# Performance work log

Measured on AMD Instinct MI355X. Metric: run time of the kernel, lower is better.

Reference implementation:

```python
import jax, jax.numpy as jnp
import numpy as np

N_NODES = 50000
N_EDGES = 800000
NFEAT, NHID, NCLASS = 512, 256, 128
N_UV = 2048


def gcn_layer(x, adj_row, adj_col, adj_val, W, b):
    # support = x @ W ; out = A @ support (sparse COO spmm) + b
    support = x @ W                                   # [N, out]
    msgs = adj_val[:, None] * support[adj_col]        # [E, out]
    out = jax.ops.segment_sum(msgs, adj_row, num_segments=N_NODES)
    return out + b


def setup_inputs() -> dict:
    key = jax.random.key(0)
    ks = jax.random.split(key, 12)
    u = jax.random.randint(ks[0], (N_UV,), 0, N_NODES)
    v = jax.random.randint(ks[1], (N_UV,), 0, N_NODES)
    x = jax.random.normal(ks[2], (N_NODES, NFEAT), dtype=jnp.float32)
    adj_row = jnp.sort(jax.random.randint(ks[3], (N_EDGES,), 0, N_NODES))
    adj_col = jax.random.randint(ks[4], (N_EDGES,), 0, N_NODES)
    adj_val = jax.random.uniform(ks[5], (N_EDGES,), dtype=jnp.float32)
    s1 = 1.0 / np.sqrt(NHID)
    s2 = 1.0 / np.sqrt(NCLASS)
    W1 = jax.random.uniform(ks[6], (NFEAT, NHID), minval=-s1, maxval=s1, dtype=jnp.float32)
    b1 = jax.random.uniform(ks[7], (NHID,), minval=-s1, maxval=s1, dtype=jnp.float32)
    W2 = jax.random.uniform(ks[8], (NHID, NCLASS), minval=-s2, maxval=s2, dtype=jnp.float32)
    b2 = jax.random.uniform(ks[9], (NCLASS,), minval=-s2, maxval=s2, dtype=jnp.float32)
    We = jax.random.normal(ks[10], (NCLASS, NCLASS), dtype=jnp.float32) * (1.0 / np.sqrt(NCLASS))
    return {"u": u, "v": v, "x": x, "adj_row": adj_row, "adj_col": adj_col,
            "adj_val": adj_val, "W1": W1, "b1": b1, "W2": W2, "b2": b2, "We": We}


def reference(u, v, x, adj_row, adj_col, adj_val, W1, b1, W2, b2, We):
    # layer 1: GCN + ReLU (dropout is identity in eval mode)
    h = jax.nn.relu(gcn_layer(x, adj_row, adj_col, adj_val, W1, b1))
    # layer 2: GCN
    z = gcn_layer(h, adj_row, adj_col, adj_val, W2, b2)          # [N, nclass]
    # edge scoring: sigmoid(w_edge(z[u]) @ z[v].T)
    zu = z[u] @ We.T                                             # [U, nclass] (nn.Linear: x @ W.T)
    zv = z[v]                                                    # [V, nclass]
    p_uv = jax.nn.sigmoid(zu @ zv.T)                             # [U, V]
    return p_uv
```

## Files before the change

### kernel.cpp

```cpp
#include <hip/hip_runtime.h>
#include <hip/hip_bf16.h>
#include <math.h>

#define N_NODES 50000
#define N_EDGES 800000
#define NFEAT   512
#define NHID    256
#define NCLASS  128
#define N_UV    2048

typedef __bf16    bf16x8 __attribute__((ext_vector_type(8)));
typedef short     s16x8  __attribute__((ext_vector_type(8)));
typedef float     f32x4  __attribute__((ext_vector_type(4)));

__device__ __forceinline__ unsigned short bf16_rn(float f) {
  unsigned u = __float_as_uint(f);
  u += 0x7fffu + ((u >> 16) & 1u);
  return (unsigned short)(u >> 16);
}
__device__ __forceinline__ float bf16_to_f(unsigned short h) {
  return __uint_as_float(((unsigned)h) << 16);
}

#define LDSPAD 40

template <bool ASPLIT, bool BSPLIT, bool SIGMOID, bool AIDX, bool BIDX>
__global__ __launch_bounds__(256, 2) void gemm_mfma_split(
    const float* __restrict__ Af,
    const unsigned short* __restrict__ Ahi, const unsigned short* __restrict__ Alo,
    const int* __restrict__ Aidx,
    const float* __restrict__ BTf,
    const unsigned short* __restrict__ BThi, const unsigned short* __restrict__ BTlo,
    const int* __restrict__ Bidx,
    float* __restrict__ C, int M, int N, int K) {
  __shared__ unsigned short sAh[128 * LDSPAD];
  __shared__ unsigned short sAl[128 * LDSPAD];
  __shared__ unsigned short sBh[128 * LDSPAD];
  __shared__ unsigned short sBl[128 * LDSPAD];

  const int tid  = threadIdx.x;
  const int lane = tid & 63;
  const int wave = tid >> 6;
  const int wm   = (wave >> 1) << 6;
  const int wn   = (wave & 1) << 6;
  const int lm   = lane & 15;
  const int quad = lane >> 4;
  const int m0   = blockIdx.y * 128;
  const int n0   = blockIdx.x * 128;

  const int r32 = tid >> 3;
  const int c32 = (tid & 7) * 4;
  const int r16 = tid >> 2;
  const int c16 = (tid & 3) * 8;

  float4 pA[4]; s16x8 pAh[2], pAl[2];
  float4 pB[4]; s16x8 pBh[2], pBl[2];

  f32x4 acc[4][4];
#pragma unroll
  for (int i = 0; i < 4; ++i)
#pragma unroll
    for (int j = 0; j < 4; ++j)
#pragma unroll
      for (int r = 0; r < 4; ++r) acc[i][j][r] = 0.f;

#define LOAD_TILE(k0)                                                          \
  do {                                                                         \
    if (ASPLIT) {                                                              \
      _Pragma("unroll") for (int p = 0; p < 4; ++p) {                          \
        const int m = m0 + p * 32 + r32;                                       \
        pA[p] = make_float4(0.f, 0.f, 0.f, 0.f);                               \
        if (m < M) {                                                           \
          const int ra = AIDX ? Aidx[m] : m;                                   \
          pA[p] = *(const float4*)&Af[(size_t)ra * K + (k0) + c32];            \
        }                                                                      \
      }                                                                        \
    } else {                                                                   \
      _Pragma("unroll") for (int p = 0; p < 2; ++p) {                          \
        const int m = m0 + p * 64 + r16;                                       \
        _Pragma("unroll") for (int e = 0; e < 8; ++e) { pAh[p][e] = 0; pAl[p][e] = 0; } \
        if (m < M) {                                                           \
          pAh[p] = *(const s16x8*)&Ahi[(size_t)m * K + (k0) + c16];            \
          pAl[p] = *(const s16x8*)&Alo[(size_t)m * K + (k0) + c16];            \
        }                                                                      \
      }                                                                        \
    }                                                                          \
    if (BSPLIT) {                                                              \
      _Pragma("unroll") for (int p = 0; p < 4; ++p) {                          \
        const int n = n0 + p * 32 + r32;                                       \
        const int rb = BIDX ? Bidx[n] : n;                                     \
        pB[p] = *(const float4*)&BTf[(size_t)rb * K + (k0) + c32];             \
      }                                                                        \
    } else {                                                                   \
      _Pragma("unroll") for (int p = 0; p < 2; ++p) {                          \
        pBh[p] = *(const s16x8*)&BThi[(size_t)(n0 + p * 64 + r16) * K + (k0) + c16]; \
        pBl[p] = *(const s16x8*)&BTlo[(size_t)(n0 + p * 64 + r16) * K + (k0) + c16]; \
      }                                                                        \
    }                                                                          \
  } while (0)

#define SPLIT4(v, hv, lv)                                                      \
  hv.x = bf16_rn(v.x); lv.x = bf16_rn(v.x - bf16_to_f(hv.x));                  \
  hv.y = bf16_rn(v.y); lv.y = bf16_rn(v.y - bf16_to_f(hv.y));                  \
  hv.z = bf16_rn(v.z); lv.z = bf16_rn(v.z - bf16_to_f(hv.z));                  \
  hv.w = bf16_rn(v.w); lv.w = bf16_rn(v.w - bf16_to_f(hv.w));

#define STORE_TILE()                                                           \
  do {                                                                         \
    if (ASPLIT) {                                                              \
      _Pragma("unroll") for (int p = 0; p < 4; ++p) {                          \
        ushort4 hv, lv; SPLIT4(pA[p], hv, lv);                                 \
        const int row = p * 32 + r32;                                          \
        *(ushort4*)&sAh[row * LDSPAD + c32] = hv;                              \
        *(ushort4*)&sAl[row * LDSPAD + c32] = lv;                              \
      }                                                                        \
    } else {                                                                   \
      _Pragma("unroll") for (int p = 0; p < 2; ++p) {                          \
        const int row = p * 64 + r16;                                          \
        *(s16x8*)&sAh[row * LDSPAD + c16] = pAh[p];                            \
        *(s16x8*)&sAl[row * LDSPAD + c16] = pAl[p];                            \
      }                                                                        \
    }                                                                          \
    if (BSPLIT) {                                                              \
      _Pragma("unroll") for (int p = 0; p < 4; ++p) {                          \
        ushort4 hv, lv; SPLIT4(pB[p], hv, lv);                                 \
        const int row = p * 32 + r32;                                          \
        *(ushort4*)&sBh[row * LDSPAD + c32] = hv;                              \
        *(ushort4*)&sBl[row * LDSPAD + c32] = lv;                              \
      }                                                                        \
    } else {                                                                   \
      _Pragma("unroll") for (int p = 0; p < 2; ++p) {                          \
        const int row = p * 64 + r16;                                          \
        *(s16x8*)&sBh[row * LDSPAD + c16] = pBh[p];                            \
        *(s16x8*)&sBl[row * LDSPAD + c16] = pBl[p];                            \
      }                                                                        \
    }                                                                          \
  } while (0)

  LOAD_TILE(0);

  for (int k0 = 0; k0 < K; k0 += 32) {
    if (k0) __syncthreads();
    STORE_TILE();
    __syncthreads();
    if (k0 + 32 < K) LOAD_TILE(k0 + 32);

    bf16x8 aH[4], aL[4], bH[4], bL[4];
#pragma unroll
    for (int i = 0; i < 4; ++i) {
      const int r = wm + i * 16 + lm;
      aH[i] = __builtin_bit_cast(bf16x8, *(const s16x8*)&sAh[r * LDSPAD + quad * 8]);
      aL[i] = __builtin_bit_cast(bf16x8, *(const s16x8*)&sAl[r * LDSPAD + quad * 8]);
    }
#pragma unroll
    for (int j = 0; j < 4; ++j) {
      const int r = wn + j * 16 + lm;
      bH[j] = __builtin_bit_cast(bf16x8, *(const s16x8*)&sBh[r * LDSPAD + quad * 8]);
      bL[j] = __builtin_bit_cast(bf16x8, *(const s16x8*)&sBl[r * LDSPAD + quad * 8]);
    }
#pragma unroll
    for (int i = 0; i < 4; ++i)
#pragma unroll
      for (int j = 0; j < 4; ++j) {
        acc[i][j] = __builtin_amdgcn_mfma_f32_16x16x32_bf16(aH[i], bH[j], acc[i][j], 0, 0, 0);
        acc[i][j] = __builtin_amdgcn_mfma_f32_16x16x32_bf16(aH[i], bL[j], acc[i][j], 0, 0, 0);
        acc[i][j] = __builtin_amdgcn_mfma_f32_16x16x32_bf16(aL[i], bH[j], acc[i][j], 0, 0, 0);
      }
  }

#pragma unroll
  for (int i = 0; i < 4; ++i)
#pragma unroll
    for (int j = 0; j < 4; ++j) {
      const int col = n0 + wn + j * 16 + lm;
#pragma unroll
      for (int r = 0; r < 4; ++r) {
        const int row = m0 + wm + i * 16 + quad * 4 + r;
        if (row < M) {
          float v = acc[i][j][r];
          if (SIGMOID) v = 1.f / (1.f + expf(-v));
          C[(size_t)row * N + col] = v;
        }
      }
    }
#undef LOAD_TILE
#undef STORE_TILE
#undef SPLIT4
}

__global__ __launch_bounds__(256) void prep_all(
    const int* __restrict__ rows, int* __restrict__ row_ptr,
    const float* __restrict__ W1, unsigned short* __restrict__ W1Thi,
    unsigned short* __restrict__ W1Tlo,
    const float* __restrict__ W2, unsigned short* __restrict__ W2Thi,
    unsigned short* __restrict__ W2Tlo) {
  const int idx = blockIdx.x * 256 + threadIdx.x;
  if (idx < N_EDGES) {
    const int r = rows[idx];
    const int rprev = (idx == 0) ? -1 : rows[idx - 1];
    for (int n = rprev + 1; n <= r; ++n) row_ptr[n] = idx;
    if (idx == N_EDGES - 1)
      for (int n = r + 1; n <= N_NODES; ++n) row_ptr[n] = N_EDGES;
  }
  if (idx < NFEAT * NHID) {
    const int n = idx / NFEAT;
    const int k = idx - n * NFEAT;
    const float f = W1[(size_t)k * NHID + n];
    const unsigned short h = bf16_rn(f);
    W1Thi[idx] = h;
    W1Tlo[idx] = bf16_rn(f - bf16_to_f(h));
  }
  if (idx < NHID * NCLASS) {
    const int n = idx / NHID;
    const int k = idx - n * NHID;
    const float f = W2[(size_t)k * NCLASS + n];
    const unsigned short h = bf16_rn(f);
    W2Thi[idx] = h;
    W2Tlo[idx] = bf16_rn(f - bf16_to_f(h));
  }
}

__global__ __launch_bounds__(256) void spmm256_split(
    const float4* __restrict__ S4, const int* __restrict__ row_ptr,
    const int* __restrict__ cols, const float* __restrict__ vals,
    const float4* __restrict__ bias4,
    unsigned short* __restrict__ outHi, unsigned short* __restrict__ outLo) {
  const int wave = threadIdx.x >> 6;
  const int lane = threadIdx.x & 63;
  const int node = blockIdx.x * 4 + wave;

  const int lo = row_ptr[node];
  const int hi = row_ptr[node + 1];

  float4 acc = make_float4(0.f, 0.f, 0.f, 0.f);
  int e = lo;
  for (; e + 8 <= hi; e += 8) {
    int c[8]; float w[8];
#pragma unroll
    for (int t = 0; t < 8; ++t) { c[t] = cols[e + t]; w[t] = vals[e + t]; }
    float4 r[8];
#pragma unroll
    for (int t = 0; t < 8; ++t) r[t] = S4[(size_t)c[t] * 64 + lane];
#pragma unroll
    for (int t = 0; t < 8; ++t) {
      acc.x = fmaf(w[t], r[t].x, acc.x); acc.y = fmaf(w[t], r[t].y, acc.y);
      acc.z = fmaf(w[t], r[t].z, acc.z); acc.w = fmaf(w[t], r[t].w, acc.w);
    }
  }
  for (; e < hi; ++e) {
    const int c = cols[e];
    const float w = vals[e];
    const float4 r = S4[(size_t)c * 64 + lane];
    acc.x = fmaf(w, r.x, acc.x); acc.y = fmaf(w, r.y, acc.y);
    acc.z = fmaf(w, r.z, acc.z); acc.w = fmaf(w, r.w, acc.w);
  }

  const float4 b = bias4[lane];
  acc.x = fmaxf(acc.x + b.x, 0.f);
  acc.y = fmaxf(acc.y + b.y, 0.f);
  acc.z = fmaxf(acc.z + b.z, 0.f);
  acc.w = fmaxf(acc.w + b.w, 0.f);

  ushort4 hv, lv;
  hv.x = bf16_rn(acc.x); lv.x = bf16_rn(acc.x - bf16_to_f(hv.x));
  hv.y = bf16_rn(acc.y); lv.y = bf16_rn(acc.y - bf16_to_f(hv.y));
  hv.z = bf16_rn(acc.z); lv.z = bf16_rn(acc.z - bf16_to_f(hv.z));
  hv.w = bf16_rn(acc.w); lv.w = bf16_rn(acc.w - bf16_to_f(hv.w));
  const size_t o = (size_t)node * NHID + lane * 4;
  *(ushort4*)&outHi[o] = hv;
  *(ushort4*)&outLo[o] = lv;
}

__global__ __launch_bounds__(256) void spmm128_f32(
    const float4* __restrict__ S4, const int* __restrict__ row_ptr,
    const int* __restrict__ cols, const float* __restrict__ vals,
    const float4* __restrict__ bias4, float4* __restrict__ out4) {
  const int wave = threadIdx.x >> 6;
  const int lane = threadIdx.x & 63;
  const int half = lane >> 5;
  const int l32  = lane & 31;
  const int node = blockIdx.x * 4 + wave;

  const int lo = row_ptr[node];
  const int hi = row_ptr[node + 1];

  float4 acc = make_float4(0.f, 0.f, 0.f, 0.f);
  int e = lo + half;
  for (; e + 6 < hi; e += 8) {
    int c[4]; float w[4];
#pragma unroll
    for (int t = 0; t < 4; ++t) { c[t] = cols[e + 2 * t]; w[t] = vals[e + 2 * t]; }
    float4 r[4];
#pragma unroll
    for (int t = 0; t < 4; ++t) r[t] = S4[(size_t)c[t] * 32 + l32];
#pragma unroll
    for (int t = 0; t < 4; ++t) {
      acc.x = fmaf(w[t], r[t].x, acc.x); acc.y = fmaf(w[t], r[t].y, acc.y);
      acc.z = fmaf(w[t], r[t].z, acc.z); acc.w = fmaf(w[t], r[t].w, acc.w);
    }
  }
  for (; e < hi; e += 2) {
    const int c = cols[e];
    const float w = vals[e];
    const float4 r = S4[(size_t)c * 32 + l32];
    acc.x = fmaf(w, r.x, acc.x); acc.y = fmaf(w, r.y, acc.y);
    acc.z = fmaf(w, r.z, acc.z); acc.w = fmaf(w, r.w, acc.w);
  }

  acc.x += __shfl_xor(acc.x, 32);
  acc.y += __shfl_xor(acc.y, 32);
  acc.z += __shfl_xor(acc.z, 32);
  acc.w += __shfl_xor(acc.w, 32);

  if (half == 0) {
    const float4 b = bias4[l32];
    acc.x += b.x; acc.y += b.y; acc.z += b.z; acc.w += b.w;
    out4[(size_t)node * 32 + l32] = acc;
  }
}

extern "C" void kernel_launch(void* const* d_in, const int* in_sizes, int n_in,
                              void* d_out, int out_size, void* d_ws, size_t ws_size,
                              hipStream_t stream) {
  const int*   u       = (const int*)  d_in[0];
  const int*   v       = (const int*)  d_in[1];
  const float* x       = (const float*)d_in[2];
  const int*   adj_row = (const int*)  d_in[3];
  const int*   adj_col = (const int*)  d_in[4];
  const float* adj_val = (const float*)d_in[5];
  const float* W1      = (const float*)d_in[6];
  const float* b1      = (const float*)d_in[7];
  const float* W2      = (const float*)d_in[8];
  const float* b2      = (const float*)d_in[9];
  const float* We      = (const float*)d_in[10];
  float* out = (float*)d_out;

  char* wsb = (char*)d_ws;
  float* S1 = (float*)wsb;
  float* S2 = (float*)wsb;
  float* Z  = (float*)(wsb + (size_t)N_NODES * NCLASS * sizeof(float));
  char* rB = wsb + (size_t)N_NODES * NHID * sizeof(float);
  unsigned short* Hhi = (unsigned short*)rB;
  unsigned short* Hlo = Hhi + (size_t)N_NODES * NHID;
  float* ZU = (float*)rB;
  unsigned short* W1Thi = (unsigned short*)out;
  unsigned short* W1Tlo = W1Thi + NHID * NFEAT;
  unsigned short* W2Thi = W1Tlo + NHID * NFEAT;
  unsigned short* W2Tlo = W2Thi + NCLASS * NHID;
  int* row_ptr = (int*)(W2Tlo + NCLASS * NHID);

  prep_all<<<(N_EDGES + 255) / 256, 256, 0, stream>>>(
      adj_row, row_ptr, W1, W1Thi, W1Tlo, W2, W2Thi, W2Tlo);

  gemm_mfma_split<true, false, false, false, false>
      <<<dim3(NHID / 128, (N_NODES + 127) / 128), 256, 0, stream>>>(
      x, nullptr, nullptr, nullptr, nullptr, W1Thi, W1Tlo, nullptr,
      S1, N_NODES, NHID, NFEAT);

  spmm256_split<<<N_NODES / 4, 256, 0, stream>>>(
      (const float4*)S1, row_ptr, adj_col, adj_val, (const float4*)b1, Hhi, Hlo);

  gemm_mfma_split<false, false, false, false, false>
      <<<dim3(NCLASS / 128, (N_NODES + 127) / 128), 256, 0, stream>>>(
      nullptr, Hhi, Hlo, nullptr, nullptr, W2Thi, W2Tlo, nullptr,
      S2, N_NODES, NCLASS, NHID);

  spmm128_f32<<<N_NODES / 4, 256, 0, stream>>>(
      (const float4*)S2, row_ptr, adj_col, adj_val, (const float4*)b2, (float4*)Z);

  gemm_mfma_split<true, true, false, true, false>
      <<<dim3(NCLASS / 128, N_UV / 128), 256, 0, stream>>>(
      Z, nullptr, nullptr, u, We, nullptr, nullptr, nullptr,
      ZU, N_UV, NCLASS, NCLASS);

  gemm_mfma_split<true, true, true, false, true>
      <<<dim3(N_UV / 128, N_UV / 128), 256, 0, stream>>>(
      ZU, nullptr, nullptr, nullptr, Z, nullptr, nullptr, v,
      out, N_UV, N_UV, NCLASS);
}
```

Baseline: 422.0 us.

## Store GEMM support outputs as 24-bit fixed point to cut SpMM gather traffic

Both support matrices (x@W1 and h@W2) are now written as packed 24-bit signed fixed-point values with a fixed scale instead of fp32. The SpMM kernels gather 12-byte packed groups and unpack them to floats, folding the scale into the edge weight. This cuts the bytes moved by the bandwidth-bound random gathers by a quarter. In exchange it adds unpack ALU work, unaligned 12-byte loads and byte-wise scattered stores in the GEMM epilogue, and it risks clamping or precision loss if values exceed the fixed range.

```diff
diff --git a/kernel.cpp b/kernel.cpp
--- a/kernel.cpp
+++ b/kernel.cpp
@@ -9,9 +9,14 @@
 #define NCLASS  128
 #define N_UV    2048
 
+#define Q24_SCALE  524288.0f
+#define Q24_INV    1.9073486328125e-6f
+
 typedef __bf16    bf16x8 __attribute__((ext_vector_type(8)));
 typedef short     s16x8  __attribute__((ext_vector_type(8)));
 typedef float     f32x4  __attribute__((ext_vector_type(4)));
+
+struct __attribute__((packed)) U3 { unsigned a, b, c; };
 
 __device__ __forceinline__ unsigned short bf16_rn(float f) {
   unsigned u = __float_as_uint(f);
@@ -21,10 +26,24 @@
 __device__ __forceinline__ float bf16_to_f(unsigned short h) {
   return __uint_as_float(((unsigned)h) << 16);
 }
+__device__ __forceinline__ void unpack24(unsigned a, unsigned b, unsigned c,
+                                         int& e0, int& e1, int& e2, int& e3) {
+  e0 = ((int)(a << 8)) >> 8;
+  e1 = ((int)((b << 16) | ((a >> 24) << 8))) >> 8;
+  e2 = ((int)((c << 24) | ((b >> 16) << 8))) >> 8;
+  e3 = ((int)c) >> 8;
+}
+__device__ __forceinline__ void pack24(float v, unsigned char* p) {
+  int q = __float2int_rn(v * Q24_SCALE);
+  q = q > 8388607 ? 8388607 : (q < -8388608 ? -8388608 : q);
+  p[0] = (unsigned char)(q & 0xFF);
+  p[1] = (unsigned char)((q >> 8) & 0xFF);
+  p[2] = (unsigned char)((q >> 16) & 0xFF);
+}
 
 #define LDSPAD 40
 
-template <bool ASPLIT, bool BSPLIT, bool SIGMOID, bool AIDX, bool BIDX>
+template <bool ASPLIT, bool BSPLIT, int OMODE, bool AIDX, bool BIDX>
 __global__ __launch_bounds__(256, 2) void gemm_mfma_split(
     const float* __restrict__ Af,
     const unsigned short* __restrict__ Ahi, const unsigned short* __restrict__ Alo,
@@ -32,7 +51,7 @@
     const float* __restrict__ BTf,
     const unsigned short* __restrict__ BThi, const unsigned short* __restrict__ BTlo,
     const int* __restrict__ Bidx,
-    float* __restrict__ C, int M, int N, int K) {
+    float* __restrict__ C, unsigned char* __restrict__ Cq, int M, int N, int K) {
   __shared__ unsigned short sAh[128 * LDSPAD];
   __shared__ unsigned short sAl[128 * LDSPAD];
   __shared__ unsigned short sBh[128 * LDSPAD];
@@ -178,8 +197,14 @@
         const int row = m0 + wm + i * 16 + quad * 4 + r;
         if (row < M) {
           float v = acc[i][j][r];
-          if (SIGMOID) v = 1.f / (1.f + expf(-v));
-          C[(size_t)row * N + col] = v;
+          if (OMODE == 1) {
+            v = 1.f / (1.f + expf(-v));
+            C[(size_t)row * N + col] = v;
+          } else if (OMODE == 2) {
+            pack24(v, Cq + ((size_t)row * N + col) * 3);
+          } else {
+            C[(size_t)row * N + col] = v;
+          }
         }
       }
     }
@@ -220,8 +245,8 @@
   }
 }
 
-__global__ __launch_bounds__(256) void spmm256_split(
-    const float4* __restrict__ S4, const int* __restrict__ row_ptr,
+__global__ __launch_bounds__(256) void spmm256_q24_split(
+    const unsigned char* __restrict__ Sq, const int* __restrict__ row_ptr,
     const int* __restrict__ cols, const float* __restrict__ vals,
     const float4* __restrict__ bias4,
     unsigned short* __restrict__ outHi, unsigned short* __restrict__ outLo) {
@@ -233,27 +258,35 @@
   const int hi = row_ptr[node + 1];
 
   float4 acc = make_float4(0.f, 0.f, 0.f, 0.f);
+
+#define ACCQ(dd, ww)                                                           \
+  do {                                                                         \
+    int e0, e1, e2, e3;                                                        \
+    unpack24((dd).a, (dd).b, (dd).c, e0, e1, e2, e3);                          \
+    const float ws = (ww) * Q24_INV;                                           \
+    acc.x = fmaf(ws, (float)e0, acc.x);                                        \
+    acc.y = fmaf(ws, (float)e1, acc.y);                                        \
+    acc.z = fmaf(ws, (float)e2, acc.z);                                        \
+    acc.w = fmaf(ws, (float)e3, acc.w);                                        \
+  } while (0)
+
   int e = lo;
   for (; e + 8 <= hi; e += 8) {
     int c[8]; float w[8];
 #pragma unroll
     for (int t = 0; t < 8; ++t) { c[t] = cols[e + t]; w[t] = vals[e + t]; }
-    float4 r[8];
-#pragma unroll
-    for (int t = 0; t < 8; ++t) r[t] = S4[(size_t)c[t] * 64 + lane];
-#pragma unroll
-    for (int t = 0; t < 8; ++t) {
-      acc.x = fmaf(w[t], r[t].x, acc.x); acc.y = fmaf(w[t], r[t].y, acc.y);
-      acc.z = fmaf(w[t], r[t].z, acc.z); acc.w = fmaf(w[t], r[t].w, acc.w);
-    }
+    U3 d[8];
+#pragma unroll
+    for (int t = 0; t < 8; ++t)
+      d[t] = *(const U3*)&Sq[(size_t)c[t] * (NHID * 3) + lane * 12];
+#pragma unroll
+    for (int t = 0; t < 8; ++t) ACCQ(d[t], w[t]);
   }
   for (; e < hi; ++e) {
-    const int c = cols[e];
-    const float w = vals[e];
-    const float4 r = S4[(size_t)c * 64 + lane];
-    acc.x = fmaf(w, r.x, acc.x); acc.y = fmaf(w, r.y, acc.y);
-    acc.z = fmaf(w, r.z, acc.z); acc.w = fmaf(w, r.w, acc.w);
-  }
+    const U3 d = *(const U3*)&Sq[(size_t)cols[e] * (NHID * 3) + lane * 12];
+    ACCQ(d, vals[e]);
+  }
+#undef ACCQ
 
   const float4 b = bias4[lane];
   acc.x = fmaxf(acc.x + b.x, 0.f);
@@ -271,10 +304,10 @@
   *(ushort4*)&outLo[o] = lv;
 }
 
-__global__ __launch_bounds__(256) void spmm128_f32(
-    const float4* __restrict__ S4, const int* __restrict__ row_ptr,
+__global__ __launch_bounds__(256) void spmm128_q24(
+    const unsigned char* __restrict__ Sq, const int* __restrict__ row_ptr,
     const int* __restrict__ cols, const float* __restrict__ vals,
-    const float4* __restrict__ bias4, float4* __restrict__ out4) {
+    const float* __restrict__ bias, float* __restrict__ Z) {
   const int wave = threadIdx.x >> 6;
   const int lane = threadIdx.x & 63;
   const int half = lane >> 5;
@@ -284,38 +317,47 @@
   const int lo = row_ptr[node];
   const int hi = row_ptr[node + 1];
 
-  float4 acc = make_float4(0.f, 0.f, 0.f, 0.f);
+  float acc[4] = {0.f, 0.f, 0.f, 0.f};
+
+#define ACCQ(dd, ww)                                                           \
+  do {                                                                         \
+    int e0, e1, e2, e3;                                                        \
+    unpack24((dd).a, (dd).b, (dd).c, e0, e1, e2, e3);                          \
+    const float ws = (ww) * Q24_INV;                                           \
+    acc[0] = fmaf(ws, (float)e0, acc[0]);                                      \
+    acc[1] = fmaf(ws, (float)e1, acc[1]);                                      \
+    acc[2] = fmaf(ws, (float)e2, acc[2]);                                      \
+    acc[3] = fmaf(ws, (float)e3, acc[3]);                                      \
+  } while (0)
+
   int e = lo + half;
   for (; e + 6 < hi; e += 8) {
     int c[4]; float w[4];
 #pragma unroll
     for (int t = 0; t < 4; ++t) { c[t] = cols[e + 2 * t]; w[t] = vals[e + 2 * t]; }
-    float4 r[4];
-#pragma unroll
-    for (int t = 0; t < 4; ++t) r[t] = S4[(size_t)c[t] * 32 + l32];
-#pragma unroll
-    for (int t = 0; t < 4; ++t) {
-      acc.x = fmaf(w[t], r[t].x, acc.x); acc.y = fmaf(w[t], r[t].y, acc.y);
-      acc.z = fmaf(w[t], r[t].z, acc.z); acc.w = fmaf(w[t], r[t].w, acc.w);
-    }
+    U3 d[4];
+#pragma unroll
+    for (int t = 0; t < 4; ++t)
+      d[t] = *(const U3*)&Sq[(size_t)c[t] * (NCLASS * 3) + l32 * 12];
+#pragma unroll
+    for (int t = 0; t < 4; ++t) ACCQ(d[t], w[t]);
   }
   for (; e < hi; e += 2) {
-    const int c = cols[e];
-    const float w = vals[e];
-    const float4 r = S4[(size_t)c * 32 + l32];
-    acc.x = fmaf(w, r.x, acc.x); acc.y = fmaf(w, r.y, acc.y);
-    acc.z = fmaf(w, r.z, acc.z); acc.w = fmaf(w, r.w, acc.w);
-  }
-
-  acc.x += __shfl_xor(acc.x, 32);
-  acc.y += __shfl_xor(acc.y, 32);
-  acc.z += __shfl_xor(acc.z, 32);
-  acc.w += __shfl_xor(acc.w, 32);
+    const U3 d = *(const U3*)&Sq[(size_t)cols[e] * (NCLASS * 3) + l32 * 12];
+    ACCQ(d, vals[e]);
+  }
+#undef ACCQ
+
+#pragma unroll
+  for (int k = 0; k < 4; ++k) acc[k] += __shfl_xor(acc[k], 32);
 
   if (half == 0) {
-    const float4 b = bias4[l32];
-    acc.x += b.x; acc.y += b.y; acc.z += b.z; acc.w += b.w;
-    out4[(size_t)node * 32 + l32] = acc;
+    float4 v;
+    v.x = acc[0] + bias[l32 * 4 + 0];
+    v.y = acc[1] + bias[l32 * 4 + 1];
+    v.z = acc[2] + bias[l32 * 4 + 2];
+    v.w = acc[3] + bias[l32 * 4 + 3];
+    *(float4*)&Z[(size_t)node * NCLASS + l32 * 4] = v;
   }
 }
 
@@ -336,9 +378,9 @@
   float* out = (float*)d_out;
 
   char* wsb = (char*)d_ws;
-  float* S1 = (float*)wsb;
-  float* S2 = (float*)wsb;
-  float* Z  = (float*)(wsb + (size_t)N_NODES * NCLASS * sizeof(float));
+  unsigned char* S1q = (unsigned char*)wsb;
+  unsigned char* S2q = (unsigned char*)wsb;
+  float* Z = (float*)(wsb + (size_t)N_NODES * NCLASS * 3);
   char* rB = wsb + (size_t)N_NODES * NHID * sizeof(float);
   unsigned short* Hhi = (unsigned short*)rB;
   unsigned short* Hlo = Hhi + (size_t)N_NODES * NHID;
@@ -352,29 +394,29 @@
   prep_all<<<(N_EDGES + 255) / 256, 256, 0, stream>>>(
       adj_row, row_ptr, W1, W1Thi, W1Tlo, W2, W2Thi, W2Tlo);
 
-  gemm_mfma_split<true, false, false, false, false>
+  gemm_mfma_split<true, false, 2, false, false>
       <<<dim3(NHID / 128, (N_NODES + 127) / 128), 256, 0, stream>>>(
       x, nullptr, nullptr, nullptr, nullptr, W1Thi, W1Tlo, nullptr,
-      S1, N_NODES, NHID, NFEAT);
-
-  spmm256_split<<<N_NODES / 4, 256, 0, stream>>>(
-      (const float4*)S1, row_ptr, adj_col, adj_val, (const float4*)b1, Hhi, Hlo);
-
-  gemm_mfma_split<false, false, false, false, false>
+      nullptr, S1q, N_NODES, NHID, NFEAT);
+
+  spmm256_q24_split<<<N_NODES / 4, 256, 0, stream>>>(
+      S1q, row_ptr, adj_col, adj_val, (const float4*)b1, Hhi, Hlo);
+
+  gemm_mfma_split<false, false, 2, false, false>
       <<<dim3(NCLASS / 128, (N_NODES + 127) / 128), 256, 0, stream>>>(
       nullptr, Hhi, Hlo, nullptr, nullptr, W2Thi, W2Tlo, nullptr,
-      S2, N_NODES, NCLASS, NHID);
-
-  spmm128_f32<<<N_NODES / 4, 256, 0, stream>>>(
-      (const float4*)S2, row_ptr, adj_col, adj_val, (const float4*)b2, (float4*)Z);
-
-  gemm_mfma_split<true, true, false, true, false>
+      nullptr, S2q, N_NODES, NCLASS, NHID);
+
+  spmm128_q24<<<N_NODES / 4, 256, 0, stream>>>(
+      S2q, row_ptr, adj_col, adj_val, b2, Z);
+
+  gemm_mfma_split<true, true, 0, true, false>
       <<<dim3(NCLASS / 128, N_UV / 128), 256, 0, stream>>>(
       Z, nullptr, nullptr, u, We, nullptr, nullptr, nullptr,
-      ZU, N_UV, NCLASS, NCLASS);
-
-  gemm_mfma_split<true, true, true, false, true>
+      ZU, nullptr, N_UV, NCLASS, NCLASS);
+
+  gemm_mfma_split<true, true, 1, false, true>
       <<<dim3(N_UV / 128, N_UV / 128), 256, 0, stream>>>(
       ZU, nullptr, nullptr, nullptr, Z, nullptr, nullptr, v,
-      out, N_UV, N_UV, NCLASS);
-}
+      out, nullptr, N_UV, N_UV, NCLASS);
+}
```

Measured after the change: 398.9 us. 5.5% less time.

## Quantize layer-1 support to 24-bit planes and aggregate layer 2 only for u/v nodes

Applied to the files above, without the earlier changes.

The layer-1 GEMM now writes its output as 24-bit fixed-point values split across three byte planes instead of fp32. The layer-1 SpMM gathers these narrower planes, which cuts gather traffic by a quarter. The layer-2 SpMM now runs only for the 4096 nodes indexed by u and v instead of all 50000, and writes a compact ZUV buffer that the final GEMMs read directly, so their index gathers are removed. The fixed-point scale clamps large values and adds quantization error; the byte-plane loads are unaligned-ish 32-bit reads from three separate arrays.

```diff
diff --git a/kernel.cpp b/kernel.cpp
--- a/kernel.cpp
+++ b/kernel.cpp
@@ -9,6 +9,9 @@
 #define NCLASS  128
 #define N_UV    2048
 
+#define Q24_SCALE  524288.0f
+#define Q24_INV    1.9073486328125e-6f
+
 typedef __bf16    bf16x8 __attribute__((ext_vector_type(8)));
 typedef short     s16x8  __attribute__((ext_vector_type(8)));
 typedef float     f32x4  __attribute__((ext_vector_type(4)));
@@ -24,15 +27,13 @@
 
 #define LDSPAD 40
 
-template <bool ASPLIT, bool BSPLIT, bool SIGMOID, bool AIDX, bool BIDX>
+template <bool ASPLIT, bool BSPLIT, int OMODE>
 __global__ __launch_bounds__(256, 2) void gemm_mfma_split(
     const float* __restrict__ Af,
     const unsigned short* __restrict__ Ahi, const unsigned short* __restrict__ Alo,
-    const int* __restrict__ Aidx,
     const float* __restrict__ BTf,
     const unsigned short* __restrict__ BThi, const unsigned short* __restrict__ BTlo,
-    const int* __restrict__ Bidx,
-    float* __restrict__ C, int M, int N, int K) {
+    float* __restrict__ C, unsigned char* __restrict__ Cq, int M, int N, int K) {
   __shared__ unsigned short sAh[128 * LDSPAD];
   __shared__ unsigned short sAl[128 * LDSPAD];
   __shared__ unsigned short sBh[128 * LDSPAD];
@@ -70,10 +71,7 @@
       _Pragma("unroll") for (int p = 0; p < 4; ++p) {                          \
         const int m = m0 + p * 32 + r32;                                       \
         pA[p] = make_float4(0.f, 0.f, 0.f, 0.f);                               \
-        if (m < M) {                                                           \
-          const int ra = AIDX ? Aidx[m] : m;                                   \
-          pA[p] = *(const float4*)&Af[(size_t)ra * K + (k0) + c32];            \
-        }                                                                      \
+        if (m < M) pA[p] = *(const float4*)&Af[(size_t)m * K + (k0) + c32];    \
       }                                                                        \
     } else {                                                                   \
       _Pragma("unroll") for (int p = 0; p < 2; ++p) {                          \
@@ -88,8 +86,7 @@
     if (BSPLIT) {                                                              \
       _Pragma("unroll") for (int p = 0; p < 4; ++p) {                          \
         const int n = n0 + p * 32 + r32;                                       \
-        const int rb = BIDX ? Bidx[n] : n;                                     \
-        pB[p] = *(const float4*)&BTf[(size_t)rb * K + (k0) + c32];             \
+        pB[p] = *(const float4*)&BTf[(size_t)n * K + (k0) + c32];              \
       }                                                                        \
     } else {                                                                   \
       _Pragma("unroll") for (int p = 0; p < 2; ++p) {                          \
@@ -168,6 +165,7 @@
       }
   }
 
+  const size_t qstride = (size_t)M * N;
 #pragma unroll
   for (int i = 0; i < 4; ++i)
 #pragma unroll
@@ -178,8 +176,19 @@
         const int row = m0 + wm + i * 16 + quad * 4 + r;
         if (row < M) {
           float v = acc[i][j][r];
-          if (SIGMOID) v = 1.f / (1.f + expf(-v));
-          C[(size_t)row * N + col] = v;
+          if (OMODE == 1) {
+            v = 1.f / (1.f + expf(-v));
+            C[(size_t)row * N + col] = v;
+          } else if (OMODE == 2) {
+            int q = __float2int_rn(v * Q24_SCALE);
+            q = q > 8388607 ? 8388607 : (q < -8388608 ? -8388608 : q);
+            const size_t o = (size_t)row * N + col;
+            Cq[o]               = (unsigned char)(q & 0xFF);
+            Cq[qstride + o]     = (unsigned char)((q >> 8) & 0xFF);
+            Cq[2 * qstride + o] = (unsigned char)((q >> 16) & 0xFF);
+          } else {
+            C[(size_t)row * N + col] = v;
+          }
         }
       }
     }
@@ -220,66 +229,86 @@
   }
 }
 
-__global__ __launch_bounds__(256) void spmm256_split(
+__global__ __launch_bounds__(256) void spmm256_q24p_split(
+    const unsigned char* __restrict__ Sq, const int* __restrict__ row_ptr,
+    const int* __restrict__ cols, const float* __restrict__ vals,
+    const float4* __restrict__ bias4,
+    unsigned short* __restrict__ outHi, unsigned short* __restrict__ outLo) {
+  const size_t MN = (size_t)N_NODES * NHID;
+  const int wave = threadIdx.x >> 6;
+  const int lane = threadIdx.x & 63;
+  const int node = blockIdx.x * 4 + wave;
+
+  const int lo = row_ptr[node];
+  const int hi = row_ptr[node + 1];
+
+  float acc[4] = {0.f, 0.f, 0.f, 0.f};
+
+#define ACCP(d0, d1, d2, ww)                                                   \
+  do {                                                                         \
+    const float ws = (ww) * Q24_INV;                                           \
+    _Pragma("unroll") for (int i = 0; i < 4; ++i) {                            \
+      const int q = ((int)((((d2) >> (8 * i)) & 0xFFu) << 24 |                 \
+                           (((d1) >> (8 * i)) & 0xFFu) << 16 |                 \
+                           (((d0) >> (8 * i)) & 0xFFu) << 8)) >> 8;            \
+      acc[i] = fmaf(ws, (float)q, acc[i]);                                     \
+    }                                                                          \
+  } while (0)
+
+  int e = lo;
+  for (; e + 8 <= hi; e += 8) {
+    int c[8]; float w[8];
+#pragma unroll
+    for (int t = 0; t < 8; ++t) { c[t] = cols[e + t]; w[t] = vals[e + t]; }
+    unsigned d0[8], d1[8], d2[8];
+#pragma unroll
+    for (int t = 0; t < 8; ++t) {
+      const size_t off = (size_t)c[t] * NHID + lane * 4;
+      d0[t] = *(const unsigned*)&Sq[off];
+      d1[t] = *(const unsigned*)&Sq[MN + off];
+      d2[t] = *(const unsigned*)&Sq[2 * MN + off];
+    }
+#pragma unroll
+    for (int t = 0; t < 8; ++t) ACCP(d0[t], d1[t], d2[t], w[t]);
+  }
+  for (; e < hi; ++e) {
+    const size_t off = (size_t)cols[e] * NHID + lane * 4;
+    const unsigned d0 = *(const unsigned*)&Sq[off];
+    const unsigned d1 = *(const unsigned*)&Sq[MN + off];
+    const unsigned d2 = *(const unsigned*)&Sq[2 * MN + off];
+    ACCP(d0, d1, d2, vals[e]);
+  }
+#undef ACCP
+
+  const float4 b = bias4[lane];
+  float4 av;
+  av.x = fmaxf(acc[0] + b.x, 0.f);
+  av.y = fmaxf(acc[1] + b.y, 0.f);
+  av.z = fmaxf(acc[2] + b.z, 0.f);
+  av.w = fmaxf(acc[3] + b.w, 0.f);
+
+  ushort4 hv, lv;
+  hv.x = bf16_rn(av.x); lv.x = bf16_rn(av.x - bf16_to_f(hv.x));
+  hv.y = bf16_rn(av.y); lv.y = bf16_rn(av.y - bf16_to_f(hv.y));
+  hv.z = bf16_rn(av.z); lv.z = bf16_rn(av.z - bf16_to_f(hv.z));
+  hv.w = bf16_rn(av.w); lv.w = bf16_rn(av.w - bf16_to_f(hv.w));
+  const size_t o = (size_t)node * NHID + lane * 4;
+  *(ushort4*)&outHi[o] = hv;
+  *(ushort4*)&outLo[o] = lv;
+}
+
+__global__ __launch_bounds__(256) void spmm128_f32_list(
     const float4* __restrict__ S4, const int* __restrict__ row_ptr,
     const int* __restrict__ cols, const float* __restrict__ vals,
     const float4* __restrict__ bias4,
-    unsigned short* __restrict__ outHi, unsigned short* __restrict__ outLo) {
-  const int wave = threadIdx.x >> 6;
-  const int lane = threadIdx.x & 63;
-  const int node = blockIdx.x * 4 + wave;
-
-  const int lo = row_ptr[node];
-  const int hi = row_ptr[node + 1];
-
-  float4 acc = make_float4(0.f, 0.f, 0.f, 0.f);
-  int e = lo;
-  for (; e + 8 <= hi; e += 8) {
-    int c[8]; float w[8];
-#pragma unroll
-    for (int t = 0; t < 8; ++t) { c[t] = cols[e + t]; w[t] = vals[e + t]; }
-    float4 r[8];
-#pragma unroll
-    for (int t = 0; t < 8; ++t) r[t] = S4[(size_t)c[t] * 64 + lane];
-#pragma unroll
-    for (int t = 0; t < 8; ++t) {
-      acc.x = fmaf(w[t], r[t].x, acc.x); acc.y = fmaf(w[t], r[t].y, acc.y);
-      acc.z = fmaf(w[t], r[t].z, acc.z); acc.w = fmaf(w[t], r[t].w, acc.w);
-    }
-  }
-  for (; e < hi; ++e) {
-    const int c = cols[e];
-    const float w = vals[e];
-    const float4 r = S4[(size_t)c * 64 + lane];
-    acc.x = fmaf(w, r.x, acc.x); acc.y = fmaf(w, r.y, acc.y);
-    acc.z = fmaf(w, r.z, acc.z); acc.w = fmaf(w, r.w, acc.w);
-  }
-
-  const float4 b = bias4[lane];
-  acc.x = fmaxf(acc.x + b.x, 0.f);
-  acc.y = fmaxf(acc.y + b.y, 0.f);
-  acc.z = fmaxf(acc.z + b.z, 0.f);
-  acc.w = fmaxf(acc.w + b.w, 0.f);
-
-  ushort4 hv, lv;
-  hv.x = bf16_rn(acc.x); lv.x = bf16_rn(acc.x - bf16_to_f(hv.x));
-  hv.y = bf16_rn(acc.y); lv.y = bf16_rn(acc.y - bf16_to_f(hv.y));
-  hv.z = bf16_rn(acc.z); lv.z = bf16_rn(acc.z - bf16_to_f(hv.z));
-  hv.w = bf16_rn(acc.w); lv.w = bf16_rn(acc.w - bf16_to_f(hv.w));
-  const size_t o = (size_t)node * NHID + lane * 4;
-  *(ushort4*)&outHi[o] = hv;
-  *(ushort4*)&outLo[o] = lv;
-}
-
-__global__ __launch_bounds__(256) void spmm128_f32(
-    const float4* __restrict__ S4, const int* __restrict__ row_ptr,
-    const int* __restrict__ cols, const float* __restrict__ vals,
-    const float4* __restrict__ bias4, float4* __restrict__ out4) {
+    const int* __restrict__ u, const int* __restrict__ v,
+    float4* __restrict__ out4) {
   const int wave = threadIdx.x >> 6;
   const int lane = threadIdx.x & 63;
   const int half = lane >> 5;
   const int l32  = lane & 31;
-  const int node = blockIdx.x * 4 + wave;
+  const int idx  = blockIdx.x * 4 + wave;
+  const int node = idx < N_UV ? u[idx] : v[idx - N_UV];
 
   const int lo = row_ptr[node];
   const int hi = row_ptr[node + 1];
@@ -315,7 +344,7 @@
   if (half == 0) {
     const float4 b = bias4[l32];
     acc.x += b.x; acc.y += b.y; acc.z += b.z; acc.w += b.w;
-    out4[(size_t)node * 32 + l32] = acc;
+    out4[(size_t)idx * 32 + l32] = acc;
   }
 }
 
@@ -336,9 +365,9 @@
   float* out = (float*)d_out;
 
   char* wsb = (char*)d_ws;
-  float* S1 = (float*)wsb;
-  float* S2 = (float*)wsb;
-  float* Z  = (float*)(wsb + (size_t)N_NODES * NCLASS * sizeof(float));
+  unsigned char* S1q = (unsigned char*)wsb;
+  float* S2  = (float*)wsb;
+  float* ZUV = (float*)(wsb + (size_t)N_NODES * NCLASS * sizeof(float));
   char* rB = wsb + (size_t)N_NODES * NHID * sizeof(float);
   unsigned short* Hhi = (unsigned short*)rB;
   unsigned short* Hlo = Hhi + (size_t)N_NODES * NHID;
@@ -352,29 +381,30 @@
   prep_all<<<(N_EDGES + 255) / 256, 256, 0, stream>>>(
       adj_row, row_ptr, W1, W1Thi, W1Tlo, W2, W2Thi, W2Tlo);
 
-  gemm_mfma_split<true, false, false, false, false>
+  gemm_mfma_split<true, false, 2>
       <<<dim3(NHID / 128, (N_NODES + 127) / 128), 256, 0, stream>>>(
-      x, nullptr, nullptr, nullptr, nullptr, W1Thi, W1Tlo, nullptr,
-      S1, N_NODES, NHID, NFEAT);
-
-  spmm256_split<<<N_NODES / 4, 256, 0, stream>>>(
-      (const float4*)S1, row_ptr, adj_col, adj_val, (const float4*)b1, Hhi, Hlo);
-
-  gemm_mfma_split<false, false, false, false, false>
+      x, nullptr, nullptr, nullptr, W1Thi, W1Tlo,
+      nullptr, S1q, N_NODES, NHID, NFEAT);
+
+  spmm256_q24p_split<<<N_NODES / 4, 256, 0, stream>>>(
+      S1q, row_ptr, adj_col, adj_val, (const float4*)b1, Hhi, Hlo);
+
+  gemm_mfma_split<false, false, 0>
       <<<dim3(NCLASS / 128, (N_NODES + 127) / 128), 256, 0, stream>>>(
-      nullptr, Hhi, Hlo, nullptr, nullptr, W2Thi, W2Tlo, nullptr,
-      S2, N_NODES, NCLASS, NHID);
-
-  spmm128_f32<<<N_NODES / 4, 256, 0, stream>>>(
-      (const float4*)S2, row_ptr, adj_col, adj_val, (const float4*)b2, (float4*)Z);
-
-  gemm_mfma_split<true, true, false, true, false>
+      nullptr, Hhi, Hlo, nullptr, W2Thi, W2Tlo,
+      S2, nullptr, N_NODES, NCLASS, NHID);
+
+  spmm128_f32_list<<<(2 * N_UV) / 4, 256, 0, stream>>>(
+      (const float4*)S2, row_ptr, adj_col, adj_val, (const float4*)b2,
+      u, v, (float4*)ZUV);
+
+  gemm_mfma_split<true, true, 0>
       <<<dim3(NCLASS / 128, N_UV / 128), 256, 0, stream>>>(
-      Z, nullptr, nullptr, u, We, nullptr, nullptr, nullptr,
-      ZU, N_UV, NCLASS, NCLASS);
-
-  gemm_mfma_split<true, true, true, false, true>
+      ZUV, nullptr, nullptr, We, nullptr, nullptr,
+      ZU, nullptr, N_UV, NCLASS, NCLASS);
+
+  gemm_mfma_split<true, true, 1>
       <<<dim3(N_UV / 128, N_UV / 128), 256, 0, stream>>>(
-      ZU, nullptr, nullptr, nullptr, Z, nullptr, nullptr, v,
-      out, N_UV, N_UV, NCLASS);
-}
+      ZU, nullptr, nullptr, ZUV + (size_t)N_UV * NCLASS, nullptr, nullptr,
+      out, nullptr, N_UV, N_UV, NCLASS);
+}
```

Result: faster. 359.6 us (-14.8%).
